# Kernel optimization log

Measured on AMD Instinct MI355X. Metric: run time of the kernel, lower is better.

## Reference

```python
import jax, jax.numpy as jnp
import numpy as np

D_MODEL = 1024
N_HEAD = 16
D_K = D_MODEL // N_HEAD
B, S = 2, 2048


def setup_inputs() -> dict:
    key = jax.random.key(0)
    ks = jax.random.split(key, 12)
    sc = 1.0 / np.sqrt(D_MODEL)
    return {
        "q": jax.random.normal(ks[0], (B, S, D_MODEL), jnp.float32),
        "k": jax.random.normal(ks[1], (B, S, D_MODEL), jnp.float32),
        "v": jax.random.normal(ks[2], (B, S, D_MODEL), jnp.float32),
        "mask": jax.random.randint(ks[3], (B, S, S), 0, 2, jnp.int32),
        # learned params (torch Linear convention: y = x @ W + b with W pre-transposed)
        "wq": jax.random.normal(ks[4], (D_MODEL, D_MODEL), jnp.float32) * sc,
        "bq": jax.random.normal(ks[5], (D_MODEL,), jnp.float32) * sc,
        "wk": jax.random.normal(ks[6], (D_MODEL, D_MODEL), jnp.float32) * sc,  # no bias
        "wv": jax.random.normal(ks[7], (D_MODEL, D_MODEL), jnp.float32) * sc,
        "bv": jax.random.normal(ks[8], (D_MODEL,), jnp.float32) * sc,
        "wf": jax.random.normal(ks[9], (D_MODEL, D_MODEL), jnp.float32) * sc,
        "bf": jax.random.normal(ks[10], (D_MODEL,), jnp.float32) * sc,
    }


def reference(q, k, v, mask, wq, bq, wk, wv, bv, wf, bf):
    bs = q.shape[0]
    temperature = jnp.asarray(D_K ** 0.5, q.dtype)
    # projections -> [b, h, s, d_k]
    qh = (q @ wq + bq).reshape(bs, -1, N_HEAD, D_K).transpose(0, 2, 1, 3)
    kh = (k @ wk).reshape(bs, -1, N_HEAD, D_K).transpose(0, 2, 1, 3)
    vh = (v @ wv + bv).reshape(bs, -1, N_HEAD, D_K).transpose(0, 2, 1, 3)
    # scores [b, h, sq, sk]
    attn = jnp.einsum("bhqd,bhkd->bhqk", qh, kh) / temperature
    m0 = (mask[:, None, :, :] == 0)  # mask==0 -> masked out, broadcast over heads
    attn = jnp.where(m0, -jnp.inf, attn)
    attn = jax.nn.softmax(attn, axis=-1)
    attn = jnp.where(m0, 0.0, attn)
    out = jnp.einsum("bhqk,bhkd->bhqd", attn, vh)
    out = out.transpose(0, 2, 1, 3).reshape(bs, -1, D_MODEL)
    return out @ wf + bf  # dropout is identity in eval mode
```

## Files before the change

kernel.cpp:

```cpp
#include <hip/hip_runtime.h>

#define D_MODEL 1024
#define NHEAD   16
#define DK      64
#define BATCH   2
#define SEQ     2048

typedef __attribute__((ext_vector_type(8))) short bf16x8;
typedef __attribute__((ext_vector_type(4))) float f32x4;

#define QSCALE 0.18033688011f

__device__ __forceinline__ unsigned short f2b(float x) {
  unsigned u = __builtin_bit_cast(unsigned, x);
  u = (u + 0x7fffu + ((u >> 16) & 1u)) >> 16;
  return (unsigned short)u;
}
__device__ __forceinline__ unsigned short f2b_rhu(float x) {
  return (unsigned short)((__builtin_bit_cast(unsigned, x) + 0x8000u) >> 16);
}
__device__ __forceinline__ int pk2(float a, float b) {
  unsigned ua = __builtin_bit_cast(unsigned, a) + 0x8000u;
  unsigned ub = __builtin_bit_cast(unsigned, b) + 0x8000u;
  return (int)__builtin_amdgcn_perm(ub, ua, 0x07060302u);
}

typedef const __attribute__((address_space(1))) void* gas_p;
typedef __attribute__((address_space(3))) void* las_p;
__device__ __forceinline__ void gll16(const void* g, void* l) {
  __builtin_amdgcn_global_load_lds((gas_p)g, (las_p)l, 16, 0, 0);
}

__global__ __launch_bounds__(256) void cast3_kernel(
    const float* __restrict__ q, const float* __restrict__ k, const float* __restrict__ v,
    unsigned short* __restrict__ qb, unsigned short* __restrict__ kb,
    unsigned short* __restrict__ vb) {
  const float* src = blockIdx.y == 0 ? q : (blockIdx.y == 1 ? k : v);
  unsigned short* dst = blockIdx.y == 0 ? qb : (blockIdx.y == 1 ? kb : vb);
  size_t i = ((size_t)blockIdx.x * 256 + threadIdx.x) * 8;
  float4 x0 = *(const float4*)&src[i];
  float4 x1 = *(const float4*)&src[i + 4];
  int4 w;
  w.x = pk2(x0.x, x0.y); w.y = pk2(x0.z, x0.w);
  w.z = pk2(x1.x, x1.y); w.w = pk2(x1.z, x1.w);
  *(int4*)&dst[i] = w;
}

__global__ __launch_bounds__(256) void wtrans_kernel(
    const float* __restrict__ wq, const float* __restrict__ wk,
    const float* __restrict__ wv, const float* __restrict__ wf,
    unsigned short* __restrict__ wqt, unsigned short* __restrict__ wkt,
    unsigned short* __restrict__ wvt, unsigned short* __restrict__ wft) {
  __shared__ float tile[64][65];
  const float* w; unsigned short* wt;
  switch (blockIdx.z) {
    case 0: w = wq; wt = wqt; break;
    case 1: w = wk; wt = wkt; break;
    case 2: w = wv; wt = wvt; break;
    default: w = wf; wt = wft; break;
  }
  int r0 = blockIdx.y * 64, c0 = blockIdx.x * 64;
  int t = threadIdx.x;
  for (int i = 0; i < 16; ++i) {
    int idx = t + i * 256; int r = idx >> 6, c = idx & 63;
    tile[r][c] = w[(size_t)(r0 + r) * D_MODEL + c0 + c];
  }
  __syncthreads();
  for (int i = 0; i < 16; ++i) {
    int idx = t + i * 256; int r = idx >> 6, c = idx & 63;
    wt[(size_t)(c0 + r) * D_MODEL + r0 + c] = f2b(tile[c][r]);
  }
}

__global__ __launch_bounds__(256) void maskpack_kernel(
    const int* __restrict__ mask, unsigned long long* __restrict__ mbits) {
  size_t gw = ((size_t)blockIdx.x * 256 + threadIdx.x) >> 6;
  int lane = threadIdx.x & 63;
  int val = mask[gw * 64 + lane];
  unsigned long long bits = __ballot(val != 0);
  if (lane == 0) mbits[gw] = bits;
}

__global__ __launch_bounds__(256) void gemm_qkv_kernel(
    const unsigned short* __restrict__ qb, const unsigned short* __restrict__ kb,
    const unsigned short* __restrict__ vb,
    const unsigned short* __restrict__ wqt, const unsigned short* __restrict__ wkt,
    const unsigned short* __restrict__ wvt,
    const float* __restrict__ bq, const float* __restrict__ bv,
    unsigned short* __restrict__ qh, unsigned short* __restrict__ kh,
    unsigned short* __restrict__ vt) {
  __shared__ unsigned short SB[16640];
  int bid = blockIdx.x;
  int xcd = bid & 7, slot = bid >> 3;
  int mi = slot & 3, zn = slot >> 2;
  int z = zn >> 3;
  int n0 = (zn & 7) * 128;
  int m0 = (mi * 8 + xcd) * 128;
  const unsigned short* A; const unsigned short* Bt;
  switch (z) {
    case 0:  A = qb; Bt = wqt; break;
    case 1:  A = kb; Bt = wkt; break;
    default: A = vb; Bt = wvt; break;
  }
  int t = threadIdx.x, lane = t & 63, wave = t >> 6;
  int l16 = lane & 15, quad = lane >> 4;
  int wm = (wave & 1) * 64, wn = (wave >> 1) * 64;
  f32x4 zero = {0.f, 0.f, 0.f, 0.f};
  f32x4 acc[4][4];
  for (int mt = 0; mt < 4; ++mt) for (int nt = 0; nt < 4; ++nt) acc[mt][nt] = zero;

  int drow = lane >> 2, dcol = (lane & 3) * 8;
  const unsigned short* asrc = A  + (size_t)(m0 + wave * 32 + drow) * D_MODEL + dcol;
  const unsigned short* bsrc = Bt + (size_t)(n0 + wave * 32 + drow) * D_MODEL + dcol;
  int dst = wave * 1024 + lane * 8;

#pragma unroll
  for (int g = 0; g < 2; ++g) {
    gll16(asrc + (size_t)(g * 16) * D_MODEL, &SB[dst + g * 512]);
    gll16(bsrc + (size_t)(g * 16) * D_MODEL, &SB[4096 + dst + g * 512]);
  }
  for (int it = 0; it < 32; ++it) {
    __syncthreads();
    if (it + 1 < 32) {
      int nb = ((it + 1) & 1) * 8192, kn = (it + 1) * 32;
#pragma unroll
      for (int g = 0; g < 2; ++g) {
        gll16(asrc + (size_t)(g * 16) * D_MODEL + kn, &SB[nb + dst + g * 512]);
        gll16(bsrc + (size_t)(g * 16) * D_MODEL + kn, &SB[nb + 4096 + dst + g * 512]);
      }
    }
    int cb = (it & 1) * 8192;
    bf16x8 a[4], b[4];
    for (int mt = 0; mt < 4; ++mt)
      a[mt] = *(const bf16x8*)&SB[cb + (wm + mt * 16 + l16) * 32 + quad * 8];
    for (int nt = 0; nt < 4; ++nt)
      b[nt] = *(const bf16x8*)&SB[cb + 4096 + (wn + nt * 16 + l16) * 32 + quad * 8];
    for (int mt = 0; mt < 4; ++mt)
      for (int nt = 0; nt < 4; ++nt)
        acc[mt][nt] = __builtin_amdgcn_mfma_f32_16x16x32_bf16(a[mt], b[nt], acc[mt][nt], 0, 0, 0);
  }

  if (z == 2) {
    __syncthreads();
#pragma unroll
    for (int nt = 0; nt < 4; ++nt) {
      int col = wn + nt * 16 + l16;
      float bb = bv[n0 + col];
      for (int mt = 0; mt < 4; ++mt)
        for (int r = 0; r < 4; ++r)
          SB[col * 130 + wm + mt * 16 + quad * 4 + r] = f2b_rhu(acc[mt][nt][r] + bb);
    }
    __syncthreads();
    int c = t >> 1, hf = t & 1;
    int colg = n0 + c, hh = colg >> 6, dd = colg & 63;
    int b_ = m0 >> 11, sbase = m0 & (SEQ - 1);
    unsigned short* dstp = vt + (((size_t)(b_ * NHEAD + hh)) * DK + dd) * SEQ + sbase + hf * 64;
#pragma unroll
    for (int j = 0; j < 8; ++j)
      *(int4*)(dstp + j * 8) = *(const int4*)&SB[c * 130 + hf * 64 + j * 8];
  } else if (z == 0) {
    for (int nt = 0; nt < 4; ++nt) {
      int col = n0 + wn + nt * 16 + l16;
      float bb = bq[col];
      int h = col >> 6, d = col & 63;
      for (int mt = 0; mt < 4; ++mt)
        for (int r = 0; r < 4; ++r) {
          int row = m0 + wm + mt * 16 + quad * 4 + r;
          int b_ = row >> 11, s = row & (SEQ - 1);
          qh[(((size_t)(b_ * NHEAD + h) * SEQ) + s) * DK + d] =
              f2b_rhu((acc[mt][nt][r] + bb) * QSCALE);
        }
    }
  } else {
    for (int nt = 0; nt < 4; ++nt) {
      int col = n0 + wn + nt * 16 + l16;
      int h = col >> 6, d = col & 63;
      for (int mt = 0; mt < 4; ++mt)
        for (int r = 0; r < 4; ++r) {
          int row = m0 + wm + mt * 16 + quad * 4 + r;
          int b_ = row >> 11, s = row & (SEQ - 1);
          kh[(((size_t)(b_ * NHEAD + h) * SEQ) + s) * DK + d] = f2b_rhu(acc[mt][nt][r]);
        }
    }
  }
}

__global__ __launch_bounds__(256) void gemm_out_kernel(
    const unsigned short* __restrict__ A, const unsigned short* __restrict__ Bt,
    const float* __restrict__ bias, float* __restrict__ out) {
  __shared__ unsigned short As[8192], Bs[8192];
  int bid = blockIdx.x;
  int xcd = bid & 7, slot = bid >> 3;
  int mi = slot & 7, n0 = (slot >> 3) * 64;
  int m0 = (mi * 8 + xcd) * 64;
  int t = threadIdx.x, lane = t & 63, wave = t >> 6;
  int l16 = lane & 15, quad = lane >> 4;
  int wm = (wave & 1) * 32, wn = (wave >> 1) * 32;
  f32x4 zero = {0.f, 0.f, 0.f, 0.f};
  f32x4 acc[2][2];
  for (int mt = 0; mt < 2; ++mt) for (int nt = 0; nt < 2; ++nt) acc[mt][nt] = zero;

  int drow = lane >> 2, dcol = (lane & 3) * 8;
  const unsigned short* asrc = A  + (size_t)(m0 + wave * 16 + drow) * D_MODEL + dcol;
  const unsigned short* bsrc = Bt + (size_t)(n0 + wave * 16 + drow) * D_MODEL + dcol;
  int dst = wave * 512 + lane * 8;

#pragma unroll
  for (int hf = 0; hf < 2; ++hf) {
    gll16(asrc + hf * 32, &As[dst + hf * 2048]);
    gll16(bsrc + hf * 32, &Bs[dst + hf * 2048]);
  }
  for (int it = 0; it < 16; ++it) {
    __syncthreads();
    if (it + 1 < 16) {
      int nb = ((it + 1) & 1) * 4096, kn = (it + 1) * 64;
#pragma unroll
      for (int hf = 0; hf < 2; ++hf) {
        gll16(asrc + kn + hf * 32, &As[nb + dst + hf * 2048]);
        gll16(bsrc + kn + hf * 32, &Bs[nb + dst + hf * 2048]);
      }
    }
    int cb = (it & 1) * 4096;
#pragma unroll
    for (int half = 0; half < 2; ++half) {
      bf16x8 a[2], b[2];
      for (int mt = 0; mt < 2; ++mt)
        a[mt] = *(const bf16x8*)&As[cb + half * 2048 + (wm + mt * 16 + l16) * 32 + quad * 8];
      for (int nt = 0; nt < 2; ++nt)
        b[nt] = *(const bf16x8*)&Bs[cb + half * 2048 + (wn + nt * 16 + l16) * 32 + quad * 8];
      for (int mt = 0; mt < 2; ++mt)
        for (int nt = 0; nt < 2; ++nt)
          acc[mt][nt] = __builtin_amdgcn_mfma_f32_16x16x32_bf16(a[mt], b[nt], acc[mt][nt], 0, 0, 0);
    }
  }
  for (int nt = 0; nt < 2; ++nt) {
    int col = n0 + wn + nt * 16 + l16;
    float bb = bias[col];
    for (int mt = 0; mt < 2; ++mt)
      for (int r = 0; r < 4; ++r) {
        int row = m0 + wm + mt * 16 + quad * 4 + r;
        out[(size_t)row * D_MODEL + col] = acc[mt][nt][r] + bb;
      }
  }
}

__global__ __launch_bounds__(256) void attn_kernel(
    const unsigned short* __restrict__ qh, const unsigned short* __restrict__ kh,
    const unsigned short* __restrict__ vt, const unsigned long long* __restrict__ mbits,
    unsigned short* __restrict__ attb) {
  __shared__ unsigned short Ks[8192];
  __shared__ unsigned short Vs[4096];
  __shared__ unsigned short Ps[4352];
  int bid = blockIdx.x;
  int xcd = bid & 7, slot = bid >> 3;
  int bh_ = 4 * xcd + (slot >> 5);
  int qt = slot & 31;
  int b = bh_ >> 4, h = bh_ & 15;
  int t = threadIdx.x, lane = t & 63, wave = t >> 6;
  int l16 = lane & 15, quad = lane >> 4;
  size_t bh = (size_t)b * NHEAD + h;

  const unsigned short* Qg = qh + (bh * SEQ + (size_t)(qt * 64 + wave * 16 + l16)) * DK;
  bf16x8 qf[2];
  qf[0] = *(const bf16x8*)&Qg[quad * 8];
  qf[1] = *(const bf16x8*)&Qg[32 + quad * 8];
  unsigned short* Pw = &Ps[wave * 1088];

  const unsigned short* Kg = kh + bh * SEQ * DK;
  const unsigned short* Vg = vt + bh * DK * SEQ;
  const unsigned long long* mrow = mbits + (size_t)b * SEQ * (SEQ / 64);
  int qrow0 = qt * 64 + wave * 16 + quad * 4;

  int drow = lane >> 2, dcol = (lane & 3) * 8;
  int dst = wave * 512 + lane * 8;
  const unsigned short* Vrow = Vg + (size_t)(wave * 16 + drow) * SEQ + dcol;

  bf16x8 ones;
#pragma unroll
  for (int i = 0; i < 8; ++i) ones[i] = (short)0x3F80;

  f32x4 zero = {0.f, 0.f, 0.f, 0.f};
  f32x4 accO[4], accRS = zero;
  for (int nt = 0; nt < 4; ++nt) accO[nt] = zero;

  {
    const unsigned short* Kt = Kg + (size_t)(wave * 16 + drow) * DK + dcol;
#pragma unroll
    for (int hf = 0; hf < 2; ++hf) gll16(Kt + hf * 32, &Ks[dst + hf * 2048]);
  }

  for (int tk = 0; tk < SEQ / 64; ++tk) {
    __syncthreads();
    if (tk + 1 < SEQ / 64) {
      int nb = ((tk + 1) & 1) * 4096;
      const unsigned short* Kt = Kg + (size_t)((tk + 1) * 64 + wave * 16 + drow) * DK + dcol;
#pragma unroll
      for (int hf = 0; hf < 2; ++hf) gll16(Kt + hf * 32, &Ks[nb + dst + hf * 2048]);
    }
#pragma unroll
    for (int hf = 0; hf < 2; ++hf) gll16(Vrow + tk * 64 + hf * 32, &Vs[dst + hf * 2048]);

    unsigned long long mw[4];
#pragma unroll
    for (int r = 0; r < 4; ++r)
      mw[r] = mrow[(size_t)(qrow0 + r) * (SEQ / 64) + tk] >> l16;

    int cb = (tk & 1) * 4096;
    f32x4 accS[4];
    for (int nt = 0; nt < 4; ++nt) accS[nt] = zero;
#pragma unroll
    for (int step = 0; step < 2; ++step)
      for (int nt = 0; nt < 4; ++nt) {
        bf16x8 bk = *(const bf16x8*)&Ks[cb + step * 2048 + (nt * 16 + l16) * 32 + quad * 8];
        accS[nt] = __builtin_amdgcn_mfma_f32_16x16x32_bf16(qf[step], bk, accS[nt], 0, 0, 0);
      }

    unsigned short pb[4][4];
#pragma unroll
    for (int r = 0; r < 4; ++r) {
      unsigned lo = (unsigned)mw[r], hi = (unsigned)(mw[r] >> 32);
#pragma unroll
      for (int nt = 0; nt < 4; ++nt) {
        unsigned halfw = (nt < 2) ? lo : hi;
        const int sh = 31 - ((nt & 1) * 16);
        float pv = __builtin_amdgcn_exp2f(accS[nt][r]);
        unsigned u = (__builtin_bit_cast(unsigned, pv) + 0x8000u) >> 16;
        int mskv = ((int)(halfw << sh)) >> 31;
        pb[r][nt] = (unsigned short)(u & (unsigned)mskv);
      }
    }

    __syncthreads();
#pragma unroll
    for (int r = 0; r < 4; ++r)
#pragma unroll
      for (int nt = 0; nt < 4; ++nt)
        Pw[(quad * 4 + r) * 68 + nt * 16 + l16] = pb[r][nt];

#pragma unroll
    for (int step = 0; step < 2; ++step) {
      short4 plo = *(const short4*)&Pw[l16 * 68 + step * 32 + quad * 8];
      short4 phi = *(const short4*)&Pw[l16 * 68 + step * 32 + quad * 8 + 4];
      bf16x8 ap = {plo.x, plo.y, plo.z, plo.w, phi.x, phi.y, phi.z, phi.w};
      accRS = __builtin_amdgcn_mfma_f32_16x16x32_bf16(ap, ones, accRS, 0, 0, 0);
      for (int nt = 0; nt < 4; ++nt) {
        bf16x8 bv_ = *(const bf16x8*)&Vs[step * 2048 + (nt * 16 + l16) * 32 + quad * 8];
        accO[nt] = __builtin_amdgcn_mfma_f32_16x16x32_bf16(ap, bv_, accO[nt], 0, 0, 0);
      }
    }
  }

  for (int r = 0; r < 4; ++r) {
    float sden = accRS[r];
    float inv = sden > 0.f ? 1.f / sden : 0.f;
    int row = qt * 64 + wave * 16 + quad * 4 + r;
    size_t ob = ((size_t)b * SEQ + row) * D_MODEL + (size_t)h * DK;
    for (int nt = 0; nt < 4; ++nt)
      attb[ob + nt * 16 + l16] = f2b_rhu(accO[nt][r] * inv);
  }
}

extern "C" void kernel_launch(void* const* d_in, const int* in_sizes, int n_in,
                              void* d_out, int out_size, void* d_ws, size_t ws_size,
                              hipStream_t stream) {
  (void)in_sizes; (void)n_in; (void)out_size; (void)ws_size;
  const float* q    = (const float*)d_in[0];
  const float* k    = (const float*)d_in[1];
  const float* v    = (const float*)d_in[2];
  const int*   mask = (const int*)d_in[3];
  const float* wq   = (const float*)d_in[4];
  const float* bq   = (const float*)d_in[5];
  const float* wk   = (const float*)d_in[6];
  const float* wv   = (const float*)d_in[7];
  const float* bv   = (const float*)d_in[8];
  const float* wf   = (const float*)d_in[9];
  const float* bf   = (const float*)d_in[10];

  char* ws = (char*)d_ws;
  unsigned short* wft  = (unsigned short*)(ws + 0);
  unsigned short* wqt  = (unsigned short*)(ws + 2097152);
  unsigned short* wkt  = (unsigned short*)(ws + 4194304);
  unsigned short* wvt  = (unsigned short*)(ws + 6291456);
  unsigned short* attb = (unsigned short*)(ws + 2097152);
  unsigned short* qhp  = (unsigned short*)(ws + 10485760);
  unsigned short* khp  = (unsigned short*)(ws + 18874368);
  unsigned short* vtp  = (unsigned short*)(ws + 27262976);
  unsigned long long* mbits = (unsigned long long*)(ws + 35651584);
  unsigned short* vb   = (unsigned short*)(ws + 36700160);
  unsigned short* qb   = (unsigned short*)d_out;
  unsigned short* kb   = (unsigned short*)d_out + 4194304;

  hipLaunchKernelGGL(cast3_kernel, dim3(2048, 3), dim3(256), 0, stream, q, k, v, qb, kb, vb);
  hipLaunchKernelGGL(wtrans_kernel, dim3(16, 16, 4), dim3(256), 0, stream,
                     wq, wk, wv, wf, wqt, wkt, wvt, wft);
  hipLaunchKernelGGL(maskpack_kernel, dim3(32768), dim3(256), 0, stream, mask, mbits);
  hipLaunchKernelGGL(gemm_qkv_kernel, dim3(768), dim3(256), 0, stream,
                     qb, kb, vb, wqt, wkt, wvt, bq, bv, qhp, khp, vtp);
  hipLaunchKernelGGL(attn_kernel, dim3(1024), dim3(256), 0, stream,
                     qhp, khp, vtp, mbits, attb);
  hipLaunchKernelGGL(gemm_out_kernel, dim3(1024), dim3(256), 0, stream,
                     attb, wft, bf, (float*)d_out);
}
```

Baseline: 288.7 us.

## Restructure attention to keep P in registers and process 128 queries per block

Each wave of the attention kernel now handles 32 query rows, so the tile has 128 queries per block and the grid is halved. Scores are computed transposed (K times Q) so that the exponentiated P tile lands directly in the register layout the 16x16x16 MFMA A-operand needs. This removes the LDS round-trip for P and the second barrier per tile. K and V tiles use an XOR-swizzled LDS layout with V double-buffered, and launch bounds request two blocks per CU. The cost is higher register pressure and fewer blocks than before, which may reduce occupancy.

```diff
diff --git a/kernel.cpp b/kernel.cpp
--- a/kernel.cpp
+++ b/kernel.cpp
@@ -7,7 +7,9 @@
 #define SEQ     2048
 
 typedef __attribute__((ext_vector_type(8))) short bf16x8;
+typedef __attribute__((ext_vector_type(4))) short bf16x4;
 typedef __attribute__((ext_vector_type(4))) float f32x4;
+typedef __attribute__((ext_vector_type(2))) int i32x2;
 
 #define QSCALE 0.18033688011f
 
@@ -24,11 +26,24 @@
   unsigned ub = __builtin_bit_cast(unsigned, b) + 0x8000u;
   return (int)__builtin_amdgcn_perm(ub, ua, 0x07060302u);
 }
+__device__ __forceinline__ int pk2u(unsigned ua, unsigned ub) {
+  return (int)__builtin_amdgcn_perm(ub + 0x8000u, ua + 0x8000u, 0x07060302u);
+}
 
 typedef const __attribute__((address_space(1))) void* gas_p;
 typedef __attribute__((address_space(3))) void* las_p;
 __device__ __forceinline__ void gll16(const void* g, void* l) {
   __builtin_amdgcn_global_load_lds((gas_p)g, (las_p)l, 16, 0, 0);
+}
+
+__device__ __forceinline__ f32x4 mfma16(bf16x4 a, bf16x4 b, f32x4 c) {
+#if __has_builtin(__builtin_amdgcn_mfma_f32_16x16x16bf16_1k)
+  return __builtin_amdgcn_mfma_f32_16x16x16bf16_1k(a, b, c, 0, 0, 0);
+#else
+  f32x4 d;
+  asm("v_mfma_f32_16x16x16_bf16 %0, %1, %2, %3" : "=v"(d) : "v"(a), "v"(b), "v"(c));
+  return d;
+#endif
 }
 
 __global__ __launch_bounds__(256) void cast3_kernel(
@@ -244,120 +259,139 @@
   }
 }
 
-__global__ __launch_bounds__(256) void attn_kernel(
+__global__ __launch_bounds__(256, 2) void attn_kernel(
     const unsigned short* __restrict__ qh, const unsigned short* __restrict__ kh,
     const unsigned short* __restrict__ vt, const unsigned long long* __restrict__ mbits,
     unsigned short* __restrict__ attb) {
   __shared__ unsigned short Ks[8192];
-  __shared__ unsigned short Vs[4096];
-  __shared__ unsigned short Ps[4352];
+  __shared__ unsigned short Vs[8192];
   int bid = blockIdx.x;
   int xcd = bid & 7, slot = bid >> 3;
-  int bh_ = 4 * xcd + (slot >> 5);
-  int qt = slot & 31;
+  int bh_ = 4 * xcd + (slot >> 4);
+  int qt = slot & 15;
   int b = bh_ >> 4, h = bh_ & 15;
   int t = threadIdx.x, lane = t & 63, wave = t >> 6;
   int l16 = lane & 15, quad = lane >> 4;
   size_t bh = (size_t)b * NHEAD + h;
 
-  const unsigned short* Qg = qh + (bh * SEQ + (size_t)(qt * 64 + wave * 16 + l16)) * DK;
-  bf16x8 qf[2];
-  qf[0] = *(const bf16x8*)&Qg[quad * 8];
-  qf[1] = *(const bf16x8*)&Qg[32 + quad * 8];
-  unsigned short* Pw = &Ps[wave * 1088];
-
   const unsigned short* Kg = kh + bh * SEQ * DK;
   const unsigned short* Vg = vt + bh * DK * SEQ;
   const unsigned long long* mrow = mbits + (size_t)b * SEQ * (SEQ / 64);
-  int qrow0 = qt * 64 + wave * 16 + quad * 4;
-
-  int drow = lane >> 2, dcol = (lane & 3) * 8;
-  int dst = wave * 512 + lane * 8;
-  const unsigned short* Vrow = Vg + (size_t)(wave * 16 + drow) * SEQ + dcol;
-
-  bf16x8 ones;
-#pragma unroll
-  for (int i = 0; i < 8; ++i) ones[i] = (short)0x3F80;
+
+  bf16x8 qf[2][2];
+#pragma unroll
+  for (int qm = 0; qm < 2; ++qm) {
+    const unsigned short* Qg =
+        qh + (bh * SEQ + (size_t)(qt * 128 + wave * 32 + qm * 16 + l16)) * DK;
+    qf[qm][0] = *(const bf16x8*)&Qg[quad * 8];
+    qf[qm][1] = *(const bf16x8*)&Qg[32 + quad * 8];
+  }
+
+  int srow = lane >> 3;
+  int schk = ((lane & 7) ^ (srow & 7)) * 8;
+  const unsigned short* ks0 = Kg + (size_t)(wave * 16 + srow) * DK + schk;
+  const unsigned short* ks1 = Kg + (size_t)(wave * 16 + 8 + srow) * DK + schk;
+  const unsigned short* vs0 = Vg + (size_t)(wave * 16 + srow) * SEQ + schk;
+  const unsigned short* vs1 = Vg + (size_t)(wave * 16 + 8 + srow) * SEQ + schk;
+  int sdst = wave * 1024 + lane * 8;
+
+  int x7 = l16 & 7;
+  int ka0 = l16 * 64 + ((quad ^ x7) * 8);
+  int ka1 = l16 * 64 + (((4 + quad) ^ x7) * 8);
+  int va[4];
+#pragma unroll
+  for (int nt = 0; nt < 4; ++nt)
+    va[nt] = l16 * 64 + (((nt * 2 + (quad >> 1)) ^ x7) * 8) + (quad & 1) * 4;
+
+  bf16x4 ones4;
+#pragma unroll
+  for (int i = 0; i < 4; ++i) ones4[i] = (short)0x3F80;
 
   f32x4 zero = {0.f, 0.f, 0.f, 0.f};
-  f32x4 accO[4], accRS = zero;
-  for (int nt = 0; nt < 4; ++nt) accO[nt] = zero;
-
-  {
-    const unsigned short* Kt = Kg + (size_t)(wave * 16 + drow) * DK + dcol;
-#pragma unroll
-    for (int hf = 0; hf < 2; ++hf) gll16(Kt + hf * 32, &Ks[dst + hf * 2048]);
-  }
+  f32x4 accO[2][4], accRS[2];
+#pragma unroll
+  for (int qm = 0; qm < 2; ++qm) {
+    accRS[qm] = zero;
+    for (int dt = 0; dt < 4; ++dt) accO[qm][dt] = zero;
+  }
+
+  gll16(ks0, &Ks[sdst]);       gll16(ks1, &Ks[sdst + 512]);
+  gll16(vs0, &Vs[sdst]);       gll16(vs1, &Vs[sdst + 512]);
 
   for (int tk = 0; tk < SEQ / 64; ++tk) {
     __syncthreads();
     if (tk + 1 < SEQ / 64) {
       int nb = ((tk + 1) & 1) * 4096;
-      const unsigned short* Kt = Kg + (size_t)((tk + 1) * 64 + wave * 16 + drow) * DK + dcol;
-#pragma unroll
-      for (int hf = 0; hf < 2; ++hf) gll16(Kt + hf * 32, &Ks[nb + dst + hf * 2048]);
-    }
-#pragma unroll
-    for (int hf = 0; hf < 2; ++hf) gll16(Vrow + tk * 64 + hf * 32, &Vs[dst + hf * 2048]);
-
-    unsigned long long mw[4];
-#pragma unroll
-    for (int r = 0; r < 4; ++r)
-      mw[r] = mrow[(size_t)(qrow0 + r) * (SEQ / 64) + tk] >> l16;
-
+      size_t ko = (size_t)(tk + 1) * 64 * DK;
+      int vo = (tk + 1) * 64;
+      gll16(ks0 + ko, &Ks[nb + sdst]);  gll16(ks1 + ko, &Ks[nb + sdst + 512]);
+      gll16(vs0 + vo, &Vs[nb + sdst]);  gll16(vs1 + vo, &Vs[nb + sdst + 512]);
+    }
     int cb = (tk & 1) * 4096;
-    f32x4 accS[4];
-    for (int nt = 0; nt < 4; ++nt) accS[nt] = zero;
-#pragma unroll
-    for (int step = 0; step < 2; ++step)
+
+    f32x4 accS[2][4];
+#pragma unroll
+    for (int qm = 0; qm < 2; ++qm)
+      for (int nt = 0; nt < 4; ++nt) accS[qm][nt] = zero;
+#pragma unroll
+    for (int step = 0; step < 2; ++step) {
+      int ka = step ? ka1 : ka0;
+#pragma unroll
       for (int nt = 0; nt < 4; ++nt) {
-        bf16x8 bk = *(const bf16x8*)&Ks[cb + step * 2048 + (nt * 16 + l16) * 32 + quad * 8];
-        accS[nt] = __builtin_amdgcn_mfma_f32_16x16x32_bf16(qf[step], bk, accS[nt], 0, 0, 0);
-      }
-
-    unsigned short pb[4][4];
-#pragma unroll
+        bf16x8 kf = *(const bf16x8*)&Ks[cb + ka + nt * 1024];
+        accS[0][nt] = __builtin_amdgcn_mfma_f32_16x16x32_bf16(kf, qf[0][step], accS[0][nt], 0, 0, 0);
+        accS[1][nt] = __builtin_amdgcn_mfma_f32_16x16x32_bf16(kf, qf[1][step], accS[1][nt], 0, 0, 0);
+      }
+    }
+
+    bf16x4 ap[2][4];
+#pragma unroll
+    for (int qm = 0; qm < 2; ++qm) {
+      int qrow = qt * 128 + wave * 32 + qm * 16 + l16;
+      unsigned long long mq = mrow[(size_t)qrow * (SEQ / 64) + tk] >> (quad * 4);
+      unsigned mlo = (unsigned)mq, mhi = (unsigned)(mq >> 32);
+#pragma unroll
+      for (int nt = 0; nt < 4; ++nt) {
+        unsigned w = (nt < 2) ? mlo : mhi;
+        unsigned pu[4];
+#pragma unroll
+        for (int r = 0; r < 4; ++r) {
+          float pv = __builtin_amdgcn_exp2f(accS[qm][nt][r]);
+          int msk = ((int)(w << (31 - ((nt & 1) * 16 + r)))) >> 31;
+          pu[r] = __builtin_bit_cast(unsigned, pv) & (unsigned)msk;
+        }
+        i32x2 wv;
+        wv[0] = pk2u(pu[0], pu[1]);
+        wv[1] = pk2u(pu[2], pu[3]);
+        ap[qm][nt] = __builtin_bit_cast(bf16x4, wv);
+      }
+#pragma unroll
+      for (int nt = 0; nt < 4; ++nt)
+        accRS[qm] = mfma16(ap[qm][nt], ones4, accRS[qm]);
+    }
+
+#pragma unroll
+    for (int nt = 0; nt < 4; ++nt) {
+      int vb_ = cb + va[nt];
+#pragma unroll
+      for (int dt = 0; dt < 4; ++dt) {
+        bf16x4 vf = *(const bf16x4*)&Vs[vb_ + dt * 1024];
+        accO[0][dt] = mfma16(ap[0][nt], vf, accO[0][dt]);
+        accO[1][dt] = mfma16(ap[1][nt], vf, accO[1][dt]);
+      }
+    }
+  }
+
+#pragma unroll
+  for (int qm = 0; qm < 2; ++qm)
     for (int r = 0; r < 4; ++r) {
-      unsigned lo = (unsigned)mw[r], hi = (unsigned)(mw[r] >> 32);
-#pragma unroll
-      for (int nt = 0; nt < 4; ++nt) {
-        unsigned halfw = (nt < 2) ? lo : hi;
-        const int sh = 31 - ((nt & 1) * 16);
-        float pv = __builtin_amdgcn_exp2f(accS[nt][r]);
-        unsigned u = (__builtin_bit_cast(unsigned, pv) + 0x8000u) >> 16;
-        int mskv = ((int)(halfw << sh)) >> 31;
-        pb[r][nt] = (unsigned short)(u & (unsigned)mskv);
-      }
-    }
-
-    __syncthreads();
-#pragma unroll
-    for (int r = 0; r < 4; ++r)
-#pragma unroll
-      for (int nt = 0; nt < 4; ++nt)
-        Pw[(quad * 4 + r) * 68 + nt * 16 + l16] = pb[r][nt];
-
-#pragma unroll
-    for (int step = 0; step < 2; ++step) {
-      short4 plo = *(const short4*)&Pw[l16 * 68 + step * 32 + quad * 8];
-      short4 phi = *(const short4*)&Pw[l16 * 68 + step * 32 + quad * 8 + 4];
-      bf16x8 ap = {plo.x, plo.y, plo.z, plo.w, phi.x, phi.y, phi.z, phi.w};
-      accRS = __builtin_amdgcn_mfma_f32_16x16x32_bf16(ap, ones, accRS, 0, 0, 0);
-      for (int nt = 0; nt < 4; ++nt) {
-        bf16x8 bv_ = *(const bf16x8*)&Vs[step * 2048 + (nt * 16 + l16) * 32 + quad * 8];
-        accO[nt] = __builtin_amdgcn_mfma_f32_16x16x32_bf16(ap, bv_, accO[nt], 0, 0, 0);
-      }
-    }
-  }
-
-  for (int r = 0; r < 4; ++r) {
-    float sden = accRS[r];
-    float inv = sden > 0.f ? 1.f / sden : 0.f;
-    int row = qt * 64 + wave * 16 + quad * 4 + r;
-    size_t ob = ((size_t)b * SEQ + row) * D_MODEL + (size_t)h * DK;
-    for (int nt = 0; nt < 4; ++nt)
-      attb[ob + nt * 16 + l16] = f2b_rhu(accO[nt][r] * inv);
-  }
+      float sden = accRS[qm][r];
+      float inv = sden > 0.f ? 1.f / sden : 0.f;
+      int row = qt * 128 + wave * 32 + qm * 16 + quad * 4 + r;
+      size_t ob = ((size_t)b * SEQ + row) * D_MODEL + (size_t)h * DK;
+      for (int dt = 0; dt < 4; ++dt)
+        attb[ob + dt * 16 + l16] = f2b_rhu(accO[qm][dt][r] * inv);
+    }
 }
 
 extern "C" void kernel_launch(void* const* d_in, const int* in_sizes, int n_in,
@@ -396,7 +430,7 @@
   hipLaunchKernelGGL(maskpack_kernel, dim3(32768), dim3(256), 0, stream, mask, mbits);
   hipLaunchKernelGGL(gemm_qkv_kernel, dim3(768), dim3(256), 0, stream,
                      qb, kb, vb, wqt, wkt, wvt, bq, bv, qhp, khp, vtp);
-  hipLaunchKernelGGL(attn_kernel, dim3(1024), dim3(256), 0, stream,
+  hipLaunchKernelGGL(attn_kernel, dim3(512), dim3(256), 0, stream,
                      qhp, khp, vtp, mbits, attb);
   hipLaunchKernelGGL(gemm_out_kernel, dim3(1024), dim3(256), 0, stream,
                      attb, wft, bf, (float*)d_out);
```

After: 280.3 us. 1.03x faster.
